# Kernel tuning notes

Measured on AMD Instinct MI355X. Metric: run time of the kernel, lower is better.

Reference implementation:

```python
import jax, jax.numpy as jnp
import numpy as np

B, C, H, W, K = 16, 1, 768, 768, 512


def setup_inputs() -> dict:
    key = jax.random.key(0)
    k1, k2, k3 = jax.random.split(key, 3)
    pre_denses = jax.random.normal(k1, (B, C, H, W), dtype=jnp.float32)
    gt_denses = jax.random.normal(k2, (B, C, H, W), dtype=jnp.float32)
    gt_cors = jax.random.randint(k3, (B, K, 2), 0, min(H, W), dtype=jnp.int32)
    return {"pre_denses": pre_denses, "gt_denses": gt_denses, "gt_cors": gt_cors}


def _peak_mask(pre):
    # The original pads by 2, shift-compares, then crops by 1; this is equivalent
    # to a zero-pad-by-1 4-neighbor local-max test at every original pixel.
    p = jnp.pad(pre, ((0, 0), (0, 0), (1, 1), (1, 1)))
    left = p[:, :, 1:-1, 2:]
    right = p[:, :, 1:-1, :-2]
    up = p[:, :, 2:, 1:-1]
    down = p[:, :, :-2, 1:-1]
    return (pre > left) & (pre > right) & (pre > up) & (pre > down)


def reference(pre_denses, gt_denses, gt_cors):
    b, c, h, w = pre_denses.shape
    # --- loss1: peak-position loss ---
    pre_mask = _peak_mask(pre_denses)  # [B,1,H,W] bool
    batch_idx = jnp.arange(b)[:, None]           # [B,1]
    ys = gt_cors[:, :, 1]                        # row index
    xs = gt_cors[:, :, 0]                        # col index
    gt_mask = jnp.zeros((b, c, h, w), dtype=bool).at[batch_idx, 0, ys, xs].set(True)
    mask1 = jnp.bitwise_xor(pre_mask, gt_mask).astype(jnp.float32)  # C_head = 1
    error = (pre_denses - gt_denses) ** 2
    l1 = jnp.mean(jnp.sum(mask1 * error, axis=(1, 2, 3)))
    # --- loss2: weighted MSE ---
    head = (gt_denses > 0).astype(jnp.float32)
    mse_mask = 5.0 * head + (1.0 - head)  # C_head=5, C_no_head=1
    l2 = jnp.mean(jnp.sum(mse_mask * error, axis=(1, 2, 3)))
    return l1 + l2
```

## Files before the change

### kernel.cpp

```cpp
#include <hip/hip_runtime.h>

#define BDIM 16
#define HDIM 768
#define WDIM 768
#define KCOR 512
constexpr int HW = HDIM * WDIM;
constexpr int TOTAL = BDIM * HW;
constexpr int TOTALQ = TOTAL / 4;

__global__ __launch_bounds__(256) void main_kernel(
    const float* __restrict__ pre,
    const float* __restrict__ gt,
    float* __restrict__ out) {

    float acc = 0.0f;
    const int nthreads = gridDim.x * blockDim.x;
    for (int q = blockIdx.x * blockDim.x + threadIdx.x; q < TOTALQ; q += nthreads) {
        const int idx = q * 4;
        const int rem = idx % HW;
        const int row = rem / WDIM;
        const int x   = rem % WDIM;

        const float4 c4 = *(const float4*)(pre + idx);
        const float4 g4 = *(const float4*)(gt + idx);
        const float  lft = (x > 0)          ? pre[idx - 1] : 0.0f;
        const float  rgt = (x + 4 < WDIM)   ? pre[idx + 4] : 0.0f;
        const float4 u4 = (row > 0)         ? *(const float4*)(pre + idx - WDIM)
                                            : make_float4(0.f, 0.f, 0.f, 0.f);
        const float4 d4 = (row < HDIM - 1)  ? *(const float4*)(pre + idx + WDIM)
                                            : make_float4(0.f, 0.f, 0.f, 0.f);

        const float c[4]  = {c4.x, c4.y, c4.z, c4.w};
        const float g[4]  = {g4.x, g4.y, g4.z, g4.w};
        const float u[4]  = {u4.x, u4.y, u4.z, u4.w};
        const float d[4]  = {d4.x, d4.y, d4.z, d4.w};
        const float lr[6] = {lft, c[0], c[1], c[2], c[3], rgt};

        #pragma unroll
        for (int j = 0; j < 4; ++j) {
            const bool peak = (c[j] > lr[j]) && (c[j] > lr[j + 2]) &&
                              (c[j] > u[j]) && (c[j] > d[j]);
            float e = c[j] - g[j];
            e *= e;
            const float wt = (g[j] > 0.0f ? 5.0f : 1.0f) + (peak ? 1.0f : 0.0f);
            acc += wt * e;
        }
    }

    #pragma unroll
    for (int off = 32; off > 0; off >>= 1) acc += __shfl_down(acc, off);

    __shared__ float lds[4];
    const int wave = threadIdx.x >> 6;
    const int lane = threadIdx.x & 63;
    if (lane == 0) lds[wave] = acc;
    __syncthreads();
    if (threadIdx.x == 0) {
        const float s = lds[0] + lds[1] + lds[2] + lds[3];
        atomicAdd(out, s * (1.0f / (float)BDIM));
    }
}

__global__ __launch_bounds__(KCOR) void corr_kernel(
    const float* __restrict__ pre,
    const float* __restrict__ gt,
    const int* __restrict__ cors,
    float* __restrict__ out) {

    __shared__ int scoord[KCOR];
    const int b = blockIdx.x;
    const int k = threadIdx.x;
    const int x = cors[(b * KCOR + k) * 2 + 0];
    const int y = cors[(b * KCOR + k) * 2 + 1];
    const int packed = y * WDIM + x;
    scoord[k] = packed;
    __syncthreads();

    bool dup = false;
    for (int k2 = 0; k2 < k; ++k2) dup |= (scoord[k2] == packed);

    float contrib = 0.0f;
    if (!dup) {
        const int idx = b * HW + packed;
        const float c = pre[idx];
        const float l = (x > 0)        ? pre[idx - 1]    : 0.0f;
        const float r = (x < WDIM - 1) ? pre[idx + 1]    : 0.0f;
        const float u = (y > 0)        ? pre[idx - WDIM] : 0.0f;
        const float d = (y < HDIM - 1) ? pre[idx + WDIM] : 0.0f;
        const bool peak = (c > l) && (c > r) && (c > u) && (c > d);
        float e = c - gt[idx];
        e *= e;
        contrib = (peak ? -1.0f : 1.0f) * e;
    }

    #pragma unroll
    for (int off = 32; off > 0; off >>= 1) contrib += __shfl_down(contrib, off);

    __shared__ float lds[8];
    const int wave = threadIdx.x >> 6;
    const int lane = threadIdx.x & 63;
    if (lane == 0) lds[wave] = contrib;
    __syncthreads();
    if (threadIdx.x == 0) {
        float s = 0.0f;
        #pragma unroll
        for (int i = 0; i < 8; ++i) s += lds[i];
        atomicAdd(out, s * (1.0f / (float)BDIM));
    }
}

extern "C" void kernel_launch(void* const* d_in, const int* in_sizes, int n_in,
                              void* d_out, int out_size, void* d_ws, size_t ws_size,
                              hipStream_t stream) {
    const float* pre  = (const float*)d_in[0];
    const float* gt   = (const float*)d_in[1];
    const int*   cors = (const int*)d_in[2];

    float* out = (float*)d_out;

    hipMemsetAsync(out, 0, sizeof(float), stream);

    main_kernel<<<1024, 256, 0, stream>>>(pre, gt, out);

    corr_kernel<<<BDIM, KCOR, 0, stream>>>(pre, gt, cors, out);
}
```

Measured before the change: 122.8 us.

## Process vertical row strips per block, reusing up/center rows in registers

Switches the main kernel from a grid-stride loop over flat float4 indices to one block per 16-row strip of an image, with 192 threads each covering one float4 column. Each thread rolls the up/center/down float4 values through registers, so every row of pre is loaded about once from global memory instead of three times. This also drops the per-iteration div/mod index math. The cost is fewer blocks (768 of 192 threads) with more serial work each and a strip-boundary halo reload.

```diff
diff --git a/kernel.cpp b/kernel.cpp
--- a/kernel.cpp
+++ b/kernel.cpp
@@ -4,31 +4,39 @@
 #define HDIM 768
 #define WDIM 768
 #define KCOR 512
+#define STRIP 16
 constexpr int HW = HDIM * WDIM;
-constexpr int TOTAL = BDIM * HW;
-constexpr int TOTALQ = TOTAL / 4;
+constexpr int QW = WDIM / 4;
+constexpr int STRIPS = HDIM / STRIP;
 
-__global__ __launch_bounds__(256) void main_kernel(
+__global__ __launch_bounds__(QW) void main_kernel(
     const float* __restrict__ pre,
     const float* __restrict__ gt,
     float* __restrict__ out) {
 
+    const int b     = blockIdx.x / STRIPS;
+    const int strip = blockIdx.x % STRIPS;
+    const int r0    = strip * STRIP;
+    const int t     = threadIdx.x;
+
+    const float* preb = pre + b * HW;
+    const float* gtb  = gt  + b * HW;
+
+    int idx = r0 * WDIM + t * 4;
+
+    float4 u4 = (r0 > 0) ? *(const float4*)(preb + idx - WDIM)
+                         : make_float4(0.f, 0.f, 0.f, 0.f);
+    float4 c4 = *(const float4*)(preb + idx);
+
     float acc = 0.0f;
-    const int nthreads = gridDim.x * blockDim.x;
-    for (int q = blockIdx.x * blockDim.x + threadIdx.x; q < TOTALQ; q += nthreads) {
-        const int idx = q * 4;
-        const int rem = idx % HW;
-        const int row = rem / WDIM;
-        const int x   = rem % WDIM;
-
-        const float4 c4 = *(const float4*)(pre + idx);
-        const float4 g4 = *(const float4*)(gt + idx);
-        const float  lft = (x > 0)          ? pre[idx - 1] : 0.0f;
-        const float  rgt = (x + 4 < WDIM)   ? pre[idx + 4] : 0.0f;
-        const float4 u4 = (row > 0)         ? *(const float4*)(pre + idx - WDIM)
-                                            : make_float4(0.f, 0.f, 0.f, 0.f);
-        const float4 d4 = (row < HDIM - 1)  ? *(const float4*)(pre + idx + WDIM)
-                                            : make_float4(0.f, 0.f, 0.f, 0.f);
+    #pragma unroll 4
+    for (int r = 0; r < STRIP; ++r) {
+        const int row = r0 + r;
+        const float4 d4 = (row < HDIM - 1) ? *(const float4*)(preb + idx + WDIM)
+                                           : make_float4(0.f, 0.f, 0.f, 0.f);
+        const float4 g4 = *(const float4*)(gtb + idx);
+        const float lft = (t > 0)      ? preb[idx - 1] : 0.0f;
+        const float rgt = (t < QW - 1) ? preb[idx + 4] : 0.0f;
 
         const float c[4]  = {c4.x, c4.y, c4.z, c4.w};
         const float g[4]  = {g4.x, g4.y, g4.z, g4.w};
@@ -45,19 +53,22 @@
             const float wt = (g[j] > 0.0f ? 5.0f : 1.0f) + (peak ? 1.0f : 0.0f);
             acc += wt * e;
         }
+
+        u4 = c4;
+        c4 = d4;
+        idx += WDIM;
     }
 
     #pragma unroll
     for (int off = 32; off > 0; off >>= 1) acc += __shfl_down(acc, off);
 
-    __shared__ float lds[4];
+    __shared__ float lds[3];
     const int wave = threadIdx.x >> 6;
     const int lane = threadIdx.x & 63;
     if (lane == 0) lds[wave] = acc;
     __syncthreads();
     if (threadIdx.x == 0) {
-        const float s = lds[0] + lds[1] + lds[2] + lds[3];
-        atomicAdd(out, s * (1.0f / (float)BDIM));
+        atomicAdd(out, (lds[0] + lds[1] + lds[2]) * (1.0f / (float)BDIM));
     }
 }
 
@@ -120,7 +131,7 @@
 
     hipMemsetAsync(out, 0, sizeof(float), stream);
 
-    main_kernel<<<1024, 256, 0, stream>>>(pre, gt, out);
+    main_kernel<<<BDIM * STRIPS, QW, 0, stream>>>(pre, gt, out);
 
     corr_kernel<<<BDIM, KCOR, 0, stream>>>(pre, gt, cors, out);
 }
```

New measurement: 116.7 us. -4.9%, faster.
